# Optimization experiments

Measured on AMD Instinct MI355X. Metric: run time of the kernel, lower is better.

Reference implementation:

```python
import jax, jax.numpy as jnp
import numpy as np

N_LAYERS = 6
N_HEADS = 16
D_MODEL = 1024
D_HEAD = D_MODEL // N_HEADS
D_FF = 4096
VOCAB = 32000
MAX_LEN = 1024
B, T = 2, 1024
NEG = -1e9
EPS = 1e-5


def layernorm(x, s, b):
    mu = jnp.mean(x, axis=-1, keepdims=True)
    var = jnp.mean(jnp.square(x - mu), axis=-1, keepdims=True)
    return (x - mu) * jax.lax.rsqrt(var + EPS) * s + b


def setup_inputs() -> dict:
    key = jax.random.key(0)
    ks = jax.random.split(key, 8)
    s = 0.02
    return {
        "idx": jax.random.randint(ks[0], (B, T), 0, VOCAB),
        "tok_emb": jax.random.normal(ks[1], (VOCAB, D_MODEL), jnp.float32) * s,
        "pos_emb": jax.random.normal(ks[2], (MAX_LEN, D_MODEL), jnp.float32) * s,
        "ln1_s": jnp.ones((N_LAYERS, D_MODEL), jnp.float32),
        "ln1_b": jnp.zeros((N_LAYERS, D_MODEL), jnp.float32),
        "qkv_w": jax.random.normal(ks[3], (N_LAYERS, D_MODEL, 3 * D_MODEL), jnp.float32) * s,
        "qkv_b": jnp.zeros((N_LAYERS, 3 * D_MODEL), jnp.float32),
        "out_w": jax.random.normal(ks[4], (N_LAYERS, D_MODEL, D_MODEL), jnp.float32) * s,
        "out_b": jnp.zeros((N_LAYERS, D_MODEL), jnp.float32),
        "ln2_s": jnp.ones((N_LAYERS, D_MODEL), jnp.float32),
        "ln2_b": jnp.zeros((N_LAYERS, D_MODEL), jnp.float32),
        "mlp_w1": jax.random.normal(ks[5], (N_LAYERS, D_MODEL, D_FF), jnp.float32) * s,
        "mlp_b1": jnp.zeros((N_LAYERS, D_FF), jnp.float32),
        "mlp_w2": jax.random.normal(ks[6], (N_LAYERS, D_FF, D_MODEL), jnp.float32) * s,
        "mlp_b2": jnp.zeros((N_LAYERS, D_MODEL), jnp.float32),
        "lnf_s": jnp.ones((D_MODEL,), jnp.float32),
        "lnf_b": jnp.zeros((D_MODEL,), jnp.float32),
        "head_w": jax.random.normal(ks[7], (D_MODEL, VOCAB), jnp.float32) * s,
    }


def reference(idx, tok_emb, pos_emb, ln1_s, ln1_b, qkv_w, qkv_b, out_w, out_b,
              ln2_s, ln2_b, mlp_w1, mlp_b1, mlp_w2, mlp_b2, lnf_s, lnf_b, head_w):
    b, t = idx.shape
    x = tok_emb[idx] + pos_emb[:t]  # [B,T,D]
    causal = jnp.tril(jnp.ones((t, t), dtype=bool))
    scale = 1.0 / np.sqrt(D_HEAD)
    for l in range(N_LAYERS):
        h = layernorm(x, ln1_s[l], ln1_b[l])
        qkv = h @ qkv_w[l] + qkv_b[l]  # [B,T,3D]
        q, k, v = jnp.split(qkv, 3, axis=-1)
        q = q.reshape(b, t, N_HEADS, D_HEAD).transpose(0, 2, 1, 3)
        k = k.reshape(b, t, N_HEADS, D_HEAD).transpose(0, 2, 1, 3)
        v = v.reshape(b, t, N_HEADS, D_HEAD).transpose(0, 2, 1, 3)
        att = jnp.einsum('bhqd,bhkd->bhqk', q, k) * scale
        att = jnp.where(causal, att, NEG)
        att = jax.nn.softmax(att, axis=-1)
        y = jnp.einsum('bhqk,bhkd->bhqd', att, v)
        y = y.transpose(0, 2, 1, 3).reshape(b, t, D_MODEL)
        x = x + (y @ out_w[l] + out_b[l])
        h = layernorm(x, ln2_s[l], ln2_b[l])
        m = jax.nn.gelu(h @ mlp_w1[l] + mlp_b1[l], approximate=False) @ mlp_w2[l] + mlp_b2[l]
        x = x + m
    x = layernorm(x, lnf_s, lnf_b)
    logits = x @ head_w  # [B,T,V]
    return logits
```

## Files before the change

kernel.cpp:

```cpp
#include <hip/hip_runtime.h>


#define T_SEQ 1024
#define NTOK  2048
#define DM    1024
#define DFF   4096
#define NH    16
#define DH    64
#define NL    6
#define VOCAB 32000

typedef short sx8 __attribute__((ext_vector_type(8)));
typedef float fx4 __attribute__((ext_vector_type(4)));
typedef unsigned short usx4 __attribute__((ext_vector_type(4)));
typedef unsigned int   uix4 __attribute__((ext_vector_type(4)));

__device__ __forceinline__ unsigned short f2bf(float f) {
  union { float f; unsigned u; } c; c.f = f;
  unsigned r = c.u + 0x7FFFu + ((c.u >> 16) & 1u);
  return (unsigned short)(r >> 16);
}
__device__ __forceinline__ float bf2f(unsigned short u) {
  union { unsigned u; float f; } c; c.u = ((unsigned)u) << 16;
  return c.f;
}
__device__ __forceinline__ unsigned cvt_pk_bf16(float lo, float hi) {
  unsigned r;
  asm("v_cvt_pk_bf16_f32 %0, %1, %2" : "=v"(r) : "v"(lo), "v"(hi));
  return r;
}

__device__ __forceinline__ void gload_lds16(const unsigned short* g, unsigned short* l) {
  __builtin_amdgcn_global_load_lds(
      (const __attribute__((address_space(1))) unsigned int*)g,
      (__attribute__((address_space(3))) unsigned int*)l, 16, 0, 0);
}

__device__ __forceinline__ int xcd_swizzle(int orig, int nwg) {
  int q = nwg >> 3, r = nwg & 7;
  int xcd = orig & 7, idx = orig >> 3;
  int base = (xcd < r) ? xcd * (q + 1) : r * (q + 1) + (xcd - r) * q;
  return base + idx;
}

__global__ __launch_bounds__(256) void k_embed_ln(const int* __restrict__ idx,
                                                  const float* __restrict__ tok,
                                                  const float* __restrict__ pos,
                                                  const float* __restrict__ g,
                                                  const float* __restrict__ b,
                                                  float* __restrict__ x,
                                                  unsigned short* __restrict__ h) {
  int token = blockIdx.x;
  int t = token & (T_SEQ - 1);
  int id = idx[token];
  int tid = threadIdx.x;
  int c = tid * 4;
  float4 tv = *(const float4*)&tok[(size_t)id * DM + c];
  float4 pv = *(const float4*)&pos[(size_t)t * DM + c];
  float4 v;
  v.x = tv.x + pv.x; v.y = tv.y + pv.y; v.z = tv.z + pv.z; v.w = tv.w + pv.w;
  *(float4*)&x[(size_t)token * DM + c] = v;
  float s = v.x + v.y + v.z + v.w;
  float q = v.x * v.x + v.y * v.y + v.z * v.z + v.w * v.w;
  for (int off = 32; off > 0; off >>= 1) {
    s += __shfl_down(s, off);
    q += __shfl_down(q, off);
  }
  __shared__ float red[8];
  int wid = tid >> 6, lane = tid & 63;
  if (lane == 0) { red[wid] = s; red[4 + wid] = q; }
  __syncthreads();
  s = red[0] + red[1] + red[2] + red[3];
  q = red[4] + red[5] + red[6] + red[7];
  float mu = s * (1.0f / DM);
  float var = q * (1.0f / DM) - mu * mu;
  float rstd = rsqrtf(var + 1e-5f);
  float4 gg = *(const float4*)&g[c];
  float4 bb = *(const float4*)&b[c];
  uint2 o;
  o.x = cvt_pk_bf16((v.x - mu) * rstd * gg.x + bb.x, (v.y - mu) * rstd * gg.y + bb.y);
  o.y = cvt_pk_bf16((v.z - mu) * rstd * gg.z + bb.z, (v.w - mu) * rstd * gg.w + bb.w);
  *(uint2*)&h[(size_t)token * DM + c] = o;
}

__global__ __launch_bounds__(256) void k_reduce_ln(const unsigned short* __restrict__ part,
                                                   float* __restrict__ x,
                                                   const float* __restrict__ g,
                                                   const float* __restrict__ b,
                                                   unsigned short* __restrict__ h) {
  int row = blockIdx.x;
  int tid = threadIdx.x;
  int c = tid * 4;
  float4 v = *(const float4*)&x[(size_t)row * DM + c];
#pragma unroll
  for (int s4 = 0; s4 < 4; ++s4) {
    usx4 p = *(const usx4*)&part[((size_t)s4 * NTOK + row) * DM + c];
    v.x += bf2f(p[0]); v.y += bf2f(p[1]); v.z += bf2f(p[2]); v.w += bf2f(p[3]);
  }
  *(float4*)&x[(size_t)row * DM + c] = v;
  float s = v.x + v.y + v.z + v.w;
  float q = v.x * v.x + v.y * v.y + v.z * v.z + v.w * v.w;
  for (int off = 32; off > 0; off >>= 1) {
    s += __shfl_down(s, off);
    q += __shfl_down(q, off);
  }
  __shared__ float red[8];
  int wid = tid >> 6, lane = tid & 63;
  if (lane == 0) { red[wid] = s; red[4 + wid] = q; }
  __syncthreads();
  s = red[0] + red[1] + red[2] + red[3];
  q = red[4] + red[5] + red[6] + red[7];
  float mu = s * (1.0f / DM);
  float var = q * (1.0f / DM) - mu * mu;
  float rstd = rsqrtf(var + 1e-5f);
  float4 gg = *(const float4*)&g[c];
  float4 bb = *(const float4*)&b[c];
  uint2 o;
  o.x = cvt_pk_bf16((v.x - mu) * rstd * gg.x + bb.x, (v.y - mu) * rstd * gg.y + bb.y);
  o.y = cvt_pk_bf16((v.z - mu) * rstd * gg.z + bb.z, (v.w - mu) * rstd * gg.w + bb.w);
  *(uint2*)&h[(size_t)row * DM + c] = o;
}

__device__ __forceinline__ void wtrans_body(const float* __restrict__ W,
                                            unsigned short* __restrict__ WT,
                                            int K, int N, int k0, int n0, int tid) {
  __shared__ float t[64][68];
#pragma unroll
  for (int i = 0; i < 4; ++i) {
    int chunk = i * 256 + tid;
    int r = chunk >> 4, c = (chunk & 15) << 2;
    float4 v = *(const float4*)&W[(size_t)(k0 + r) * N + n0 + c];
    t[r][c] = v.x; t[r][c + 1] = v.y; t[r][c + 2] = v.z; t[r][c + 3] = v.w;
  }
  __syncthreads();
#pragma unroll
  for (int i = 0; i < 4; ++i) {
    int chunk = i * 256 + tid;
    int n = chunk >> 4, c = (chunk & 15) << 2;
    uint2 o;
    o.x = cvt_pk_bf16(t[c][n], t[c + 1][n]);
    o.y = cvt_pk_bf16(t[c + 2][n], t[c + 3][n]);
    *(uint2*)&WT[(size_t)(n0 + n) * K + k0 + c] = o;
  }
}

__global__ __launch_bounds__(256) void k_wtrans(const float* __restrict__ W,
                                                unsigned short* __restrict__ WT,
                                                int K, int N) {
  wtrans_body(W, WT, K, N, blockIdx.x * 64, blockIdx.y * 64, threadIdx.x);
}

__global__ __launch_bounds__(256) void k_wtrans4(const float* __restrict__ W0,
                                                 const float* __restrict__ W1,
                                                 const float* __restrict__ W2,
                                                 const float* __restrict__ W3,
                                                 unsigned short* __restrict__ T0,
                                                 unsigned short* __restrict__ T1,
                                                 unsigned short* __restrict__ T2,
                                                 unsigned short* __restrict__ T3) {
  int id = blockIdx.x;
  const float* W; unsigned short* WT; int K, N, lid;
  if (id < 768)       { W = W0; WT = T0; K = 1024; N = 3072; lid = id; }
  else if (id < 1024) { W = W1; WT = T1; K = 1024; N = 1024; lid = id - 768; }
  else if (id < 2048) { W = W2; WT = T2; K = 1024; N = 4096; lid = id - 1024; }
  else                { W = W3; WT = T3; K = 4096; N = 1024; lid = id - 2048; }
  int kb = K >> 6;
  wtrans_body(W, WT, K, N, (lid % kb) * 64, (lid / kb) * 64, threadIdx.x);
}

template <int EPI>
__global__ __launch_bounds__(256) void k_gemm(const unsigned short* __restrict__ A,
                                              const unsigned short* __restrict__ BT,
                                              const float* __restrict__ bias,
                                              unsigned short* __restrict__ part,
                                              unsigned short* __restrict__ outb,
                                              float* __restrict__ outf,
                                              int N, int K, int NT, int KS) {
  __shared__ unsigned short As[2][128 * 64];
  __shared__ unsigned short Bs[2][128 * 64];
  int tid = threadIdx.x;
  int wid = tid >> 6, lane = tid & 63;
  int lr = lane & 15, lg = lane >> 4;

  int id = xcd_swizzle(blockIdx.x, gridDim.x);
  int mt = id & 15;
  int rest = id >> 4;
  int nt = rest % NT;
  int ks = rest / NT;
  int m0 = mt * 128, n0 = nt * 128;
  int Kslice = K / KS;
  int kbeg = ks * Kslice;
  int nk = Kslice >> 6;

  int wm = (wid >> 1) * 64, wn = (wid & 1) * 64;

  fx4 acc[4][4] = {};

#define GSTAGE(buf, kt)                                                         \
  {                                                                             \
    _Pragma("unroll")                                                           \
    for (int i = 0; i < 4; ++i) {                                               \
      int chunk = i * 256 + tid;                                                \
      int r = chunk >> 3, slot = chunk & 7;                                     \
      int c = ((slot ^ (r & 7)) << 3);                                          \
      gload_lds16(&A[(size_t)(m0 + r) * K + (kt) + c], &As[buf][chunk << 3]);   \
      gload_lds16(&BT[(size_t)(n0 + r) * K + (kt) + c], &Bs[buf][chunk << 3]);  \
    }                                                                           \
  }

  GSTAGE(0, kbeg);
  for (int ik = 0; ik < nk; ++ik) {
    int cur = ik & 1;
    if (ik + 1 < nk) {
      GSTAGE(cur ^ 1, kbeg + (ik + 1) * 64);
      asm volatile("s_waitcnt vmcnt(8)" ::: "memory");
    } else {
      asm volatile("s_waitcnt vmcnt(0)" ::: "memory");
    }
    __builtin_amdgcn_sched_barrier(0);
    __builtin_amdgcn_s_barrier();
    __builtin_amdgcn_sched_barrier(0);
#pragma unroll
    for (int kk = 0; kk < 2; ++kk) {
      int slotz = (kk * 4 + lg) ^ (lr & 7);
      sx8 fa[4], fb[4];
#pragma unroll
      for (int mi = 0; mi < 4; ++mi)
        fa[mi] = *(const sx8*)&As[cur][(wm + mi * 16 + lr) * 64 + slotz * 8];
#pragma unroll
      for (int ni = 0; ni < 4; ++ni)
        fb[ni] = *(const sx8*)&Bs[cur][(wn + ni * 16 + lr) * 64 + slotz * 8];
#pragma unroll
      for (int mi = 0; mi < 4; ++mi)
#pragma unroll
        for (int ni = 0; ni < 4; ++ni)
          acc[mi][ni] = __builtin_amdgcn_mfma_f32_16x16x32_bf16(fb[ni], fa[mi], acc[mi][ni], 0, 0, 0);
    }
    asm volatile("s_waitcnt lgkmcnt(0)" ::: "memory");
    __builtin_amdgcn_sched_barrier(0);
    __builtin_amdgcn_s_barrier();
  }
#undef GSTAGE

#pragma unroll
  for (int ni = 0; ni < 4; ++ni) {
    int col0 = n0 + wn + ni * 16 + lg * 4;
    float4 bv = {0.f, 0.f, 0.f, 0.f};
    if (bias && ks == 0) bv = *(const float4*)&bias[col0];
#pragma unroll
    for (int mi = 0; mi < 4; ++mi) {
      int row = m0 + wm + mi * 16 + lr;
      float v0 = acc[mi][ni][0] + bv.x;
      float v1 = acc[mi][ni][1] + bv.y;
      float v2 = acc[mi][ni][2] + bv.z;
      float v3 = acc[mi][ni][3] + bv.w;
      if constexpr (EPI == 0) {
        int bb = row >> 10, tt = row & 1023;
        if (col0 < 2048) {
          int which = col0 >> 10;
          int hc = col0 & 1023;
          uint2 o = {cvt_pk_bf16(v0, v1), cvt_pk_bf16(v2, v3)};
          *(uint2*)&outb[(size_t)which * NTOK * DM +
                         (((size_t)bb * NH + (hc >> 6)) * T_SEQ + tt) * DH + (hc & 63)] = o;
        } else {
          int dc = col0 - 2048;
          unsigned short* vt = outb + (size_t)2 * NTOK * DM;
          size_t base = (((size_t)bb * NH + (dc >> 6)) * DH + (dc & 63)) * T_SEQ + tt;
          vt[base] = f2bf(v0);
          vt[base + T_SEQ] = f2bf(v1);
          vt[base + 2 * T_SEQ] = f2bf(v2);
          vt[base + 3 * T_SEQ] = f2bf(v3);
        }
      } else if constexpr (EPI == 1) {
        float g0 = 0.5f * v0 * (1.0f + erff(v0 * 0.70710678f));
        float g1 = 0.5f * v1 * (1.0f + erff(v1 * 0.70710678f));
        float g2 = 0.5f * v2 * (1.0f + erff(v2 * 0.70710678f));
        float g3 = 0.5f * v3 * (1.0f + erff(v3 * 0.70710678f));
        uint2 o = {cvt_pk_bf16(g0, g1), cvt_pk_bf16(g2, g3)};
        *(uint2*)&outb[(size_t)row * N + col0] = o;
      } else {
        uint2 o = {cvt_pk_bf16(v0, v1), cvt_pk_bf16(v2, v3)};
        *(uint2*)&part[((size_t)ks * NTOK + row) * DM + col0] = o;
      }
    }
  }
}

#define LDSUB(buf, ab, kk) (lds + (((buf) * 2 + (ab)) * 2 + (kk)) * 8192)

__device__ __forceinline__ void stage_half(const unsigned short* g, int rowstride,
                                           unsigned short* ldsbase, int tid, int k0) {
#pragma unroll
  for (int r = 0; r < 2; ++r) {
    int chunk = r * 512 + tid;
    int row = chunk >> 2, slot = chunk & 3;
    gload_lds16(g + (size_t)row * rowstride + k0 + ((slot ^ ((row >> 1) & 3)) << 3),
                ldsbase + (chunk << 3));
  }
}

__global__ __launch_bounds__(512, 2) void k_gemm256(const unsigned short* __restrict__ A,
                                                    const unsigned short* __restrict__ BT,
                                                    float* __restrict__ outf,
                                                    int N, int K) {
  __shared__ unsigned short lds[8 * 8192];
  int tid = threadIdx.x;
  int wid = tid >> 6, lane = tid & 63;
  int lr = lane & 15, lg = lane >> 4;
  int wm2 = wid >> 2, wn4 = wid & 3;
  int id = xcd_swizzle(blockIdx.x, gridDim.x);
  int mt = id & 7, nt = id >> 3;
  int m0 = mt * 256, n0 = nt * 256;
  const unsigned short* Ab = A + (size_t)m0 * K;
  const unsigned short* Bb = BT + (size_t)n0 * K;
  int NIT = K >> 7;
  int swz = (lg ^ ((lr >> 1) & 3)) << 3;
  float* obase = outf + (size_t)(m0 + wm2 * 128 + lr) * N + n0 + wn4 * 64 + lg * 4;

  fx4 acc[8][4] = {};

  stage_half(Ab, K, LDSUB(0, 0, 0), tid, 0);
  stage_half(Bb, K, LDSUB(0, 1, 0), tid, 0);
  stage_half(Ab, K, LDSUB(0, 0, 1), tid, 32);
  stage_half(Bb, K, LDSUB(0, 1, 1), tid, 32);
  stage_half(Ab, K, LDSUB(1, 0, 0), tid, 64);
  stage_half(Bb, K, LDSUB(1, 1, 0), tid, 64);
  stage_half(Ab, K, LDSUB(1, 0, 1), tid, 96);
  asm volatile("s_waitcnt vmcnt(6)" ::: "memory");
  __builtin_amdgcn_s_barrier();

#define PHASE(BUF, KK, NHH, LOADA, STG, VMW)                                         \
  {                                                                                  \
    if (LOADA) {                                                                     \
      const unsigned short* sA = LDSUB(BUF, 0, KK);                                  \
      _Pragma("unroll")                                                              \
      for (int mi = 0; mi < 8; ++mi)                                                 \
        fa[mi] = *(const sx8*)&sA[(wm2 * 128 + mi * 16 + lr) * 32 + swz];            \
    }                                                                                \
    {                                                                                \
      const unsigned short* sB = LDSUB(BUF, 1, KK);                                  \
      _Pragma("unroll")                                                              \
      for (int j = 0; j < 2; ++j)                                                    \
        fb[j] = *(const sx8*)&sB[(wn4 * 64 + (NHH) * 32 + j * 16 + lr) * 32 + swz];  \
    }                                                                                \
    STG;                                                                             \
    VMW;                                                                             \
    __builtin_amdgcn_sched_barrier(0);                                               \
    __builtin_amdgcn_s_barrier();                                                    \
    asm volatile("s_waitcnt lgkmcnt(0)" ::: "memory");                               \
    __builtin_amdgcn_sched_barrier(0);                                               \
    __builtin_amdgcn_s_setprio(1);                                                   \
    _Pragma("unroll")                                                                \
    for (int mi = 0; mi < 8; ++mi) {                                                 \
      acc[mi][(NHH) * 2 + 0] = __builtin_amdgcn_mfma_f32_16x16x32_bf16(              \
          fb[0], fa[mi], acc[mi][(NHH) * 2 + 0], 0, 0, 0);                           \
      acc[mi][(NHH) * 2 + 1] = __builtin_amdgcn_mfma_f32_16x16x32_bf16(              \
          fb[1], fa[mi], acc[mi][(NHH) * 2 + 1], 0, 0, 0);                           \
    }                                                                                \
    __builtin_amdgcn_s_setprio(0);                                                   \
    __builtin_amdgcn_sched_barrier(0);                                               \
    __builtin_amdgcn_s_barrier();                                                    \
  }

  for (int it = 0; it < NIT; ++it) {
    bool st = (it < NIT - 1);
    bool last = (it == NIT - 1);
    int t1k = (2 * it + 1) * 64;
    int t2k = (2 * it + 2) * 64;
    int t3k = (2 * it + 3) * 64;
    sx8 fa[8], fb[2];

    PHASE(0, 0, 0, true,
          { stage_half(Bb, K, LDSUB(1, 1, 1), tid, t1k + 32); }, {});
    PHASE(0, 0, 1, false,
          { if (st) stage_half(Ab, K, LDSUB(0, 0, 0), tid, t2k); }, {});
    PHASE(0, 1, 0, true,
          { if (st) stage_half(Bb, K, LDSUB(0, 1, 0), tid, t2k); }, {});
    PHASE(0, 1, 1, false,
          { if (st) stage_half(Ab, K, LDSUB(0, 0, 1), tid, t2k + 32); },
          { if (last) { asm volatile("s_waitcnt vmcnt(0)" ::: "memory"); }
            else      { asm volatile("s_waitcnt vmcnt(6)" ::: "memory"); } });
    PHASE(1, 0, 0, true,
          { if (st) stage_half(Bb, K, LDSUB(0, 1, 1), tid, t2k + 32); }, {});
    PHASE(1, 0, 1, false,
          { if (st) stage_half(Ab, K, LDSUB(1, 0, 0), tid, t3k); }, {});
    PHASE(1, 1, 0, true,
          { if (st) stage_half(Bb, K, LDSUB(1, 1, 0), tid, t3k); }, {});
    if (last) {
#pragma unroll
      for (int mi = 0; mi < 8; ++mi) {
        *(float4*)(obase + (size_t)mi * 16 * N) =
            (float4){acc[mi][0][0], acc[mi][0][1], acc[mi][0][2], acc[mi][0][3]};
        *(float4*)(obase + (size_t)mi * 16 * N + 16) =
            (float4){acc[mi][1][0], acc[mi][1][1], acc[mi][1][2], acc[mi][1][3]};
      }
    }
    PHASE(1, 1, 1, false,
          { if (st) stage_half(Ab, K, LDSUB(1, 0, 1), tid, t3k + 32); },
          { if (!last) { asm volatile("s_waitcnt vmcnt(6)" ::: "memory"); } });
  }
#undef PHASE

#pragma unroll
  for (int mi = 0; mi < 8; ++mi) {
    *(float4*)(obase + (size_t)mi * 16 * N + 32) =
        (float4){acc[mi][2][0], acc[mi][2][1], acc[mi][2][2], acc[mi][2][3]};
    *(float4*)(obase + (size_t)mi * 16 * N + 48) =
        (float4){acc[mi][3][0], acc[mi][3][1], acc[mi][3][2], acc[mi][3][3]};
  }
}

__global__ __launch_bounds__(256) void k_attn(const unsigned short* __restrict__ gq,
                                              const unsigned short* __restrict__ gk,
                                              const unsigned short* __restrict__ gvt,
                                              unsigned short* __restrict__ y) {
  __shared__ unsigned short Ks[128 * 64];
  __shared__ unsigned short Vt[64 * 128];
  __shared__ unsigned short Pw[4][16 * 136];
  int id = xcd_swizzle(blockIdx.x, gridDim.x);
  int bh = id >> 4, qt = 15 - (id & 15);
  int tid = threadIdx.x, wid = tid >> 6, lane = tid & 63;
  int lr = lane & 15, lg = lane >> 4;
  int q0 = qt * 64 + wid * 16;
  int qg = q0 + lr;
  const float SCL = 0.125f * 1.44269504f;

  sx8 qf[2];
  {
    const unsigned short* qp = gq + ((size_t)bh * T_SEQ + qg) * DH + lg * 8;
    qf[0] = *(const sx8*)qp;
    qf[1] = *(const sx8*)(qp + 32);
  }

  fx4 yacc[4] = {};
  float mrun = -1e30f, lrun = 0.f;

  int jmax = qt >> 1;
  for (int j = 0; j <= jmax; ++j) {
    int kt0 = j * 128;
    __syncthreads();
#pragma unroll
    for (int i = 0; i < 4; ++i) {
      int chunk = i * 256 + tid;
      {
        int r = chunk >> 3, s = chunk & 7;
        gload_lds16(&gk[((size_t)bh * T_SEQ + kt0 + r) * DH + ((s ^ (r & 7)) << 3)],
                    &Ks[chunk << 3]);
      }
      {
        int r = chunk >> 4, s = chunk & 15;
        gload_lds16(&gvt[((size_t)bh * DH + r) * T_SEQ + kt0 + ((s ^ (r & 15)) << 3)],
                    &Vt[chunk << 3]);
      }
    }
    __syncthreads();

    fx4 st[8] = {};
#pragma unroll
    for (int kk = 0; kk < 2; ++kk) {
      int slotz = (kk * 4 + lg) ^ (lr & 7);
#pragma unroll
      for (int mi = 0; mi < 8; ++mi) {
        sx8 kb = *(const sx8*)&Ks[(mi * 16 + lr) * 64 + slotz * 8];
        st[mi] = __builtin_amdgcn_mfma_f32_16x16x32_bf16(kb, qf[kk], st[mi], 0, 0, 0);
      }
    }

    float pvv[8][4];
    float pmax = -1e30f;
    if (j < jmax) {
#pragma unroll
      for (int mi = 0; mi < 8; ++mi)
#pragma unroll
        for (int rg = 0; rg < 4; ++rg) {
          float val = st[mi][rg] * SCL;
          pvv[mi][rg] = val;
          pmax = fmaxf(pmax, val);
        }
    } else {
#pragma unroll
      for (int mi = 0; mi < 8; ++mi)
#pragma unroll
        for (int rg = 0; rg < 4; ++rg) {
          float val = st[mi][rg] * SCL;
          if ((kt0 + mi * 16 + lg * 4 + rg) > qg) val = -1e30f;
          pvv[mi][rg] = val;
          pmax = fmaxf(pmax, val);
        }
    }
    pmax = fmaxf(pmax, __shfl_xor(pmax, 16));
    pmax = fmaxf(pmax, __shfl_xor(pmax, 32));
    if (!__all(pmax <= mrun + 11.5f)) {
      float mnew = fmaxf(mrun, pmax);
      float sc = exp2f(mrun - mnew);
      lrun *= sc;
#pragma unroll
      for (int dt = 0; dt < 4; ++dt)
#pragma unroll
        for (int rg = 0; rg < 4; ++rg) yacc[dt][rg] *= sc;
      mrun = mnew;
    }
    float ps = 0.f;
#pragma unroll
    for (int mi = 0; mi < 8; ++mi)
#pragma unroll
      for (int rg = 0; rg < 4; ++rg) {
        float e = exp2f(pvv[mi][rg] - mrun);
        pvv[mi][rg] = e;
        ps += e;
      }
    ps += __shfl_xor(ps, 16);
    ps += __shfl_xor(ps, 32);
    lrun += ps;

#pragma unroll
    for (int mi = 0; mi < 8; ++mi)
#pragma unroll
      for (int rp = 0; rp < 2; ++rp) {
        unsigned pk = cvt_pk_bf16(pvv[mi][rp * 2], pvv[mi][rp * 2 + 1]);
        *(unsigned*)&Pw[wid][lr * 136 + mi * 16 + lg * 4 + rp * 2] = pk;
      }

#pragma unroll
    for (int kk = 0; kk < 4; ++kk) {
      sx8 pa = *(const sx8*)&Pw[wid][lr * 136 + kk * 32 + lg * 8];
      int slotz = (kk * 4 + lg) ^ lr;
#pragma unroll
      for (int dt = 0; dt < 4; ++dt) {
        sx8 vb = *(const sx8*)&Vt[(dt * 16 + lr) * 128 + slotz * 8];
        yacc[dt] = __builtin_amdgcn_mfma_f32_16x16x32_bf16(vb, pa, yacc[dt], 0, 0, 0);
      }
    }
  }

  float inv = 1.0f / lrun;
  int tok = (bh >> 4) * T_SEQ + qg;
  int colbase = (bh & 15) * DH;
#pragma unroll
  for (int dt = 0; dt < 4; ++dt) {
    uint2 o;
    o.x = cvt_pk_bf16(yacc[dt][0] * inv, yacc[dt][1] * inv);
    o.y = cvt_pk_bf16(yacc[dt][2] * inv, yacc[dt][3] * inv);
    *(uint2*)&y[(size_t)tok * DM + colbase + dt * 16 + lg * 4] = o;
  }
}

extern "C" void kernel_launch(void* const* d_in, const int* in_sizes, int n_in,
                              void* d_out, int out_size, void* d_ws, size_t ws_size,
                              hipStream_t stream) {
  (void)in_sizes; (void)n_in; (void)out_size; (void)ws_size;
  const int*   idx     = (const int*)d_in[0];
  const float* tok_emb = (const float*)d_in[1];
  const float* pos_emb = (const float*)d_in[2];
  const float* ln1_s   = (const float*)d_in[3];
  const float* ln1_b   = (const float*)d_in[4];
  const float* qkv_w   = (const float*)d_in[5];
  const float* qkv_b   = (const float*)d_in[6];
  const float* out_w   = (const float*)d_in[7];
  const float* out_b   = (const float*)d_in[8];
  const float* ln2_s   = (const float*)d_in[9];
  const float* ln2_b   = (const float*)d_in[10];
  const float* mlp_w1  = (const float*)d_in[11];
  const float* mlp_b1  = (const float*)d_in[12];
  const float* mlp_w2  = (const float*)d_in[13];
  const float* mlp_b2  = (const float*)d_in[14];
  const float* lnf_s   = (const float*)d_in[15];
  const float* lnf_b   = (const float*)d_in[16];
  const float* head_w  = (const float*)d_in[17];

  char* p = (char*)d_ws;
  float* x          = (float*)p;          p += (size_t)NTOK * DM * 4;
  unsigned short* h = (unsigned short*)p; p += (size_t)NTOK * DM * 2;
  unsigned short* qkvb = (unsigned short*)p; p += (size_t)3 * NTOK * DM * 2;
  unsigned short* yb = (unsigned short*)p; p += (size_t)NTOK * DM * 2;
  unsigned short* m1 = (unsigned short*)p; p += (size_t)NTOK * DFF * 2;
  unsigned short* wt = (unsigned short*)p;
  unsigned short* wtq  = wt;
  unsigned short* wto  = wt + (size_t)3 * 1024 * 1024;
  unsigned short* wtm1 = wt + (size_t)4 * 1024 * 1024;
  unsigned short* wtm2 = wt + (size_t)8 * 1024 * 1024;
  unsigned short* part = (unsigned short*)(p + 32 * 1024 * 1024);

  dim3 blk(256);

  k_embed_ln<<<NTOK, blk, 0, stream>>>(idx, tok_emb, pos_emb, ln1_s, ln1_b, x, h);

  for (int l = 0; l < NL; ++l) {
    k_wtrans4<<<3072, blk, 0, stream>>>(qkv_w + (size_t)l * DM * 3 * DM,
                                        out_w + (size_t)l * DM * DM,
                                        mlp_w1 + (size_t)l * DM * DFF,
                                        mlp_w2 + (size_t)l * DFF * DM,
                                        wtq, wto, wtm1, wtm2);
    k_gemm<0><<<16 * 24, blk, 0, stream>>>(h, wtq, qkv_b + l * 3 * DM,
                                           nullptr, qkvb, nullptr, 3 * DM, DM, 24, 1);
    k_attn<<<512, blk, 0, stream>>>(qkvb, qkvb + (size_t)NTOK * DM,
                                    qkvb + (size_t)2 * NTOK * DM, yb);
    k_gemm<2><<<16 * 8 * 4, blk, 0, stream>>>(yb, wto, out_b + l * DM,
                                              part, nullptr, nullptr, DM, DM, 8, 4);
    k_reduce_ln<<<NTOK, blk, 0, stream>>>(part, x, ln2_s + l * DM, ln2_b + l * DM, h);
    k_gemm<1><<<16 * 32, blk, 0, stream>>>(h, wtm1, mlp_b1 + l * DFF,
                                           nullptr, m1, nullptr, DFF, DM, 32, 1);
    k_gemm<2><<<16 * 8 * 4, blk, 0, stream>>>(m1, wtm2, mlp_b2 + l * DM,
                                              part, nullptr, nullptr, DM, DFF, 8, 4);
    if (l < NL - 1)
      k_reduce_ln<<<NTOK, blk, 0, stream>>>(part, x, ln1_s + (l + 1) * DM, ln1_b + (l + 1) * DM, h);
    else
      k_reduce_ln<<<NTOK, blk, 0, stream>>>(part, x, lnf_s, lnf_b, h);
  }

  k_wtrans<<<dim3(DM / 64, VOCAB / 64), blk, 0, stream>>>(head_w, wt, DM, VOCAB);
  k_gemm256<<<1000, 512, 0, stream>>>(h, wt, (float*)d_out, VOCAB, DM);
}
```

Baseline: 1.090 ms.

## Merge GEMM half-N phases into four full-tile phases per iteration

Restructures the pipelined bf16 GEMM main loop from eight half-N phases to four phases, each loading all A and B fragments and issuing 32 MFMAs per wave. A and B halves are now staged together, with adjusted vmcnt waits, and the early store of the first output half is dropped so all outputs are written at the end. This halves the number of barriers per K-step and gives longer MFMA bursts between syncs, at the cost of more live fragment registers and less fine-grained overlap of global loads with compute.

```diff
diff --git a/kernel.cpp b/kernel.cpp
--- a/kernel.cpp
+++ b/kernel.cpp
@@ -325,24 +325,19 @@
   stage_half(Bb, K, LDSUB(0, 1, 1), tid, 32);
   stage_half(Ab, K, LDSUB(1, 0, 0), tid, 64);
   stage_half(Bb, K, LDSUB(1, 1, 0), tid, 64);
-  stage_half(Ab, K, LDSUB(1, 0, 1), tid, 96);
-  asm volatile("s_waitcnt vmcnt(6)" ::: "memory");
+  asm volatile("s_waitcnt vmcnt(8)" ::: "memory");
   __builtin_amdgcn_s_barrier();
 
-#define PHASE(BUF, KK, NHH, LOADA, STG, VMW)                                         \
+#define PH(BUF, KK, STG, VMW)                                                        \
   {                                                                                  \
-    if (LOADA) {                                                                     \
-      const unsigned short* sA = LDSUB(BUF, 0, KK);                                  \
-      _Pragma("unroll")                                                              \
-      for (int mi = 0; mi < 8; ++mi)                                                 \
-        fa[mi] = *(const sx8*)&sA[(wm2 * 128 + mi * 16 + lr) * 32 + swz];            \
-    }                                                                                \
-    {                                                                                \
-      const unsigned short* sB = LDSUB(BUF, 1, KK);                                  \
-      _Pragma("unroll")                                                              \
-      for (int j = 0; j < 2; ++j)                                                    \
-        fb[j] = *(const sx8*)&sB[(wn4 * 64 + (NHH) * 32 + j * 16 + lr) * 32 + swz];  \
-    }                                                                                \
+    const unsigned short* sA = LDSUB(BUF, 0, KK);                                    \
+    _Pragma("unroll")                                                                \
+    for (int mi = 0; mi < 8; ++mi)                                                   \
+      fa[mi] = *(const sx8*)&sA[(wm2 * 128 + mi * 16 + lr) * 32 + swz];              \
+    const unsigned short* sB = LDSUB(BUF, 1, KK);                                    \
+    _Pragma("unroll")                                                                \
+    for (int q = 0; q < 4; ++q)                                                      \
+      fb[q] = *(const sx8*)&sB[(wn4 * 64 + q * 16 + lr) * 32 + swz];                 \
     STG;                                                                             \
     VMW;                                                                             \
     __builtin_amdgcn_sched_barrier(0);                                               \
@@ -351,12 +346,11 @@
     __builtin_amdgcn_sched_barrier(0);                                               \
     __builtin_amdgcn_s_setprio(1);                                                   \
     _Pragma("unroll")                                                                \
-    for (int mi = 0; mi < 8; ++mi) {                                                 \
-      acc[mi][(NHH) * 2 + 0] = __builtin_amdgcn_mfma_f32_16x16x32_bf16(              \
-          fb[0], fa[mi], acc[mi][(NHH) * 2 + 0], 0, 0, 0);                           \
-      acc[mi][(NHH) * 2 + 1] = __builtin_amdgcn_mfma_f32_16x16x32_bf16(              \
-          fb[1], fa[mi], acc[mi][(NHH) * 2 + 1], 0, 0, 0);                           \
-    }                                                                                \
+    for (int mi = 0; mi < 8; ++mi)                                                   \
+      _Pragma("unroll")                                                              \
+      for (int q = 0; q < 4; ++q)                                                    \
+        acc[mi][q] = __builtin_amdgcn_mfma_f32_16x16x32_bf16(fb[q], fa[mi],          \
+                                                             acc[mi][q], 0, 0, 0);   \
     __builtin_amdgcn_s_setprio(0);                                                   \
     __builtin_amdgcn_sched_barrier(0);                                               \
     __builtin_amdgcn_s_barrier();                                                    \
@@ -364,49 +358,39 @@
 
   for (int it = 0; it < NIT; ++it) {
     bool st = (it < NIT - 1);
-    bool last = (it == NIT - 1);
-    int t1k = (2 * it + 1) * 64;
-    int t2k = (2 * it + 2) * 64;
-    int t3k = (2 * it + 3) * 64;
-    sx8 fa[8], fb[2];
-
-    PHASE(0, 0, 0, true,
-          { stage_half(Bb, K, LDSUB(1, 1, 1), tid, t1k + 32); }, {});
-    PHASE(0, 0, 1, false,
-          { if (st) stage_half(Ab, K, LDSUB(0, 0, 0), tid, t2k); }, {});
-    PHASE(0, 1, 0, true,
-          { if (st) stage_half(Bb, K, LDSUB(0, 1, 0), tid, t2k); }, {});
-    PHASE(0, 1, 1, false,
-          { if (st) stage_half(Ab, K, LDSUB(0, 0, 1), tid, t2k + 32); },
-          { if (last) { asm volatile("s_waitcnt vmcnt(0)" ::: "memory"); }
-            else      { asm volatile("s_waitcnt vmcnt(6)" ::: "memory"); } });
-    PHASE(1, 0, 0, true,
-          { if (st) stage_half(Bb, K, LDSUB(0, 1, 1), tid, t2k + 32); }, {});
-    PHASE(1, 0, 1, false,
-          { if (st) stage_half(Ab, K, LDSUB(1, 0, 0), tid, t3k); }, {});
-    PHASE(1, 1, 0, true,
-          { if (st) stage_half(Bb, K, LDSUB(1, 1, 0), tid, t3k); }, {});
-    if (last) {
-#pragma unroll
-      for (int mi = 0; mi < 8; ++mi) {
-        *(float4*)(obase + (size_t)mi * 16 * N) =
-            (float4){acc[mi][0][0], acc[mi][0][1], acc[mi][0][2], acc[mi][0][3]};
-        *(float4*)(obase + (size_t)mi * 16 * N + 16) =
-            (float4){acc[mi][1][0], acc[mi][1][1], acc[mi][1][2], acc[mi][1][3]};
-      }
-    }
-    PHASE(1, 1, 1, false,
-          { if (st) stage_half(Ab, K, LDSUB(1, 0, 1), tid, t3k + 32); },
-          { if (!last) { asm volatile("s_waitcnt vmcnt(6)" ::: "memory"); } });
-  }
-#undef PHASE
+    int b_k = (2 * it + 1) * 64;
+    int a2k = (2 * it + 2) * 64;
+    int b2k = (2 * it + 3) * 64;
+    sx8 fa[8], fb[4];
+
+    PH(0, 0,
+       { stage_half(Ab, K, LDSUB(1, 0, 1), tid, b_k + 32);
+         stage_half(Bb, K, LDSUB(1, 1, 1), tid, b_k + 32); },
+       { asm volatile("s_waitcnt vmcnt(8)" ::: "memory"); });
+    PH(0, 1,
+       { if (st) { stage_half(Ab, K, LDSUB(0, 0, 0), tid, a2k);
+                   stage_half(Bb, K, LDSUB(0, 1, 0), tid, a2k); } },
+       { if (st) { asm volatile("s_waitcnt vmcnt(8)" ::: "memory"); }
+         else    { asm volatile("s_waitcnt vmcnt(4)" ::: "memory"); } });
+    PH(1, 0,
+       { if (st) { stage_half(Ab, K, LDSUB(0, 0, 1), tid, a2k + 32);
+                   stage_half(Bb, K, LDSUB(0, 1, 1), tid, a2k + 32); } },
+       { if (st) { asm volatile("s_waitcnt vmcnt(8)" ::: "memory"); }
+         else    { asm volatile("s_waitcnt vmcnt(0)" ::: "memory"); } });
+    PH(1, 1,
+       { if (st) { stage_half(Ab, K, LDSUB(1, 0, 0), tid, b2k);
+                   stage_half(Bb, K, LDSUB(1, 1, 0), tid, b2k); } },
+       { if (st) { asm volatile("s_waitcnt vmcnt(8)" ::: "memory"); } });
+  }
+#undef PH
 
 #pragma unroll
   for (int mi = 0; mi < 8; ++mi) {
-    *(float4*)(obase + (size_t)mi * 16 * N + 32) =
-        (float4){acc[mi][2][0], acc[mi][2][1], acc[mi][2][2], acc[mi][2][3]};
-    *(float4*)(obase + (size_t)mi * 16 * N + 48) =
-        (float4){acc[mi][3][0], acc[mi][3][1], acc[mi][3][2], acc[mi][3][3]};
+#pragma unroll
+    for (int nj = 0; nj < 4; ++nj) {
+      float4 o = {acc[mi][nj][0], acc[mi][nj][1], acc[mi][nj][2], acc[mi][nj][3]};
+      *(float4*)(obase + (size_t)mi * 16 * N + nj * 16) = o;
+    }
   }
 }
 
```

Result: no change. 1.102 ms (+1.0%).

## Prefetch next K/V tiles in attention to overlap loads with compute

Applied to the files above, without the earlier changes.

Restructures the attention inner loop so the next K tile is loaded into shared memory while the P·V MFMAs run, and the next V tile is loaded after P·V finishes, overlapping with the following QK^T. It replaces the two full __syncthreads per iteration with explicit vmcnt/lgkmcnt waits and s_barrier calls. This aims to hide global-to-LDS load latency. The cost is fragile, hand-placed wait counts that must match the number of outstanding loads.

```diff
diff --git a/kernel.cpp b/kernel.cpp
--- a/kernel.cpp
+++ b/kernel.cpp
@@ -425,6 +425,27 @@
   int qg = q0 + lr;
   const float SCL = 0.125f * 1.44269504f;
 
+#define STAGE_K(kt0)                                                                  \
+  {                                                                                   \
+    _Pragma("unroll")                                                                 \
+    for (int i = 0; i < 4; ++i) {                                                     \
+      int chunk = i * 256 + tid;                                                      \
+      int r = chunk >> 3, s = chunk & 7;                                              \
+      gload_lds16(&gk[((size_t)bh * T_SEQ + (kt0) + r) * DH + ((s ^ (r & 7)) << 3)],  \
+                  &Ks[chunk << 3]);                                                   \
+    }                                                                                 \
+  }
+#define STAGE_V(kt0)                                                                  \
+  {                                                                                   \
+    _Pragma("unroll")                                                                 \
+    for (int i = 0; i < 4; ++i) {                                                     \
+      int chunk = i * 256 + tid;                                                      \
+      int r = chunk >> 4, s = chunk & 15;                                             \
+      gload_lds16(&gvt[((size_t)bh * DH + r) * T_SEQ + (kt0) + ((s ^ (r & 15)) << 3)],\
+                  &Vt[chunk << 3]);                                                   \
+    }                                                                                 \
+  }
+
   sx8 qf[2];
   {
     const unsigned short* qp = gq + ((size_t)bh * T_SEQ + qg) * DH + lg * 8;
@@ -435,25 +456,16 @@
   fx4 yacc[4] = {};
   float mrun = -1e30f, lrun = 0.f;
 
+  STAGE_K(0);
+  STAGE_V(0);
+  asm volatile("s_waitcnt vmcnt(4)" ::: "memory");
+  __builtin_amdgcn_sched_barrier(0);
+  __builtin_amdgcn_s_barrier();
+
   int jmax = qt >> 1;
   for (int j = 0; j <= jmax; ++j) {
     int kt0 = j * 128;
-    __syncthreads();
-#pragma unroll
-    for (int i = 0; i < 4; ++i) {
-      int chunk = i * 256 + tid;
-      {
-        int r = chunk >> 3, s = chunk & 7;
-        gload_lds16(&gk[((size_t)bh * T_SEQ + kt0 + r) * DH + ((s ^ (r & 7)) << 3)],
-                    &Ks[chunk << 3]);
-      }
-      {
-        int r = chunk >> 4, s = chunk & 15;
-        gload_lds16(&gvt[((size_t)bh * DH + r) * T_SEQ + kt0 + ((s ^ (r & 15)) << 3)],
-                    &Vt[chunk << 3]);
-      }
-    }
-    __syncthreads();
+    bool more = (j < jmax);
 
     fx4 st[8] = {};
 #pragma unroll
@@ -521,6 +533,13 @@
         *(unsigned*)&Pw[wid][lr * 136 + mi * 16 + lg * 4 + rp * 2] = pk;
       }
 
+    asm volatile("s_waitcnt vmcnt(0)" ::: "memory");
+    __builtin_amdgcn_sched_barrier(0);
+    __builtin_amdgcn_s_barrier();
+    __builtin_amdgcn_sched_barrier(0);
+
+    if (more) STAGE_K(kt0 + 128);
+
 #pragma unroll
     for (int kk = 0; kk < 4; ++kk) {
       sx8 pa = *(const sx8*)&Pw[wid][lr * 136 + kk * 32 + lg * 8];
@@ -531,7 +550,20 @@
         yacc[dt] = __builtin_amdgcn_mfma_f32_16x16x32_bf16(vb, pa, yacc[dt], 0, 0, 0);
       }
     }
-  }
+
+    if (more) {
+      asm volatile("s_waitcnt lgkmcnt(0)" ::: "memory");
+      __builtin_amdgcn_sched_barrier(0);
+      __builtin_amdgcn_s_barrier();
+      __builtin_amdgcn_sched_barrier(0);
+      STAGE_V(kt0 + 128);
+      asm volatile("s_waitcnt vmcnt(4)" ::: "memory");
+      __builtin_amdgcn_sched_barrier(0);
+      __builtin_amdgcn_s_barrier();
+    }
+  }
+#undef STAGE_K
+#undef STAGE_V
 
   float inv = 1.0f / lrun;
   int tok = (bh >> 4) * T_SEQ + qg;
```

Result: no change. 1.089 ms (-0.2%).
